# Optimization experiments

Hardware: AMD Instinct MI355X
Metric: run time of the kernel (lower is better)

## Reference

```python
import jax, jax.numpy as jnp
import numpy as np

NUM_NODES = 100000
NUM_FEATS = 128
NUM_EDGES = 3200000
NUM_HEADS = 4


def setup_inputs() -> dict:
    key = jax.random.key(0)
    k1, k2, k3, k4 = jax.random.split(key, 4)
    x = jax.random.normal(k1, (NUM_NODES, NUM_FEATS), dtype=jnp.float32)
    # torch Linear: weight [out, in], bias [out]; scale weight down so q.k scores stay sane
    W = jax.random.normal(k2, (2 * NUM_HEADS * NUM_FEATS, NUM_FEATS), dtype=jnp.float32) * 0.05
    b = jax.random.normal(k3, (2 * NUM_HEADS * NUM_FEATS,), dtype=jnp.float32) * 0.05
    edge_index = jax.random.randint(k4, (2, NUM_EDGES), 0, NUM_NODES, dtype=jnp.int64)
    return {"x": x, "W": W, "b": b, "edge_index": edge_index}


def reference(x, W, b, edge_index):
    N = x.shape[0]
    H, F = NUM_HEADS, NUM_FEATS
    # qk_lin: [N, 2*H*F]
    qk = x @ W.T + b
    # 'L (h hdim) -> L h hdim' with hdim=2F, then split along hdim into q, k
    qk = qk.reshape(N, H, 2 * F)
    q = qk[..., :F]   # [N, H, F]
    k = qk[..., F:]   # [N, H, F]
    row, col = edge_index[0], edge_index[1]
    # per-edge dot-product score per head (NOTE: original never applies self.scale)
    scores = jnp.einsum('ehf,ehf->eh', q[row], k[col])  # [E, H]
    # sparse softmax over columns within each (head, row) segment
    seg_max = jax.ops.segment_max(scores, row, num_segments=N)  # [N, H]
    ex = jnp.exp(scores - seg_max[row])
    seg_sum = jax.ops.segment_sum(ex, row, num_segments=N)      # [N, H]
    attn = ex / seg_sum[row]                                    # [E, H]
    # average over heads (torch.sparse.sum over head dim / num_heads)
    return attn.mean(axis=1)                                    # [E] per-edge values
```

## Files before the change

### kernel.cpp

```cpp
#include <hip/hip_runtime.h>
#include <hip/hip_fp16.h>

#define N_NODES 100000
#define N_FEATS 128
#define N_EDGES 3200000
#define N_HEADS 4
#define QK_HALFS ((size_t)N_NODES * 512)
#define CAP 64
#define GROUPS 8
#define ROWS_PER_G (N_NODES / GROUPS)
#define STRIPS (N_NODES / 16)
#define NBLK ((N_NODES + 255) / 256)
#define XCONV_BLKS 6250
#define WCONV_BLKS 64
#define GEMM3_BLKS 6250

typedef _Float16 half2t __attribute__((ext_vector_type(2)));
typedef _Float16 fp16x8 __attribute__((ext_vector_type(8)));
typedef float f32x4 __attribute__((ext_vector_type(4)));
struct alignas(16) H8 { half2t h[4]; };
union F4H8 { f32x4 f; H8 h; };

__device__ inline float fdot2(half2t a, half2t b, float c) {
#if __has_builtin(__builtin_amdgcn_fdot2)
  return __builtin_amdgcn_fdot2(a, b, c, false);
#else
  return c + (float)a.x * (float)b.x + (float)a.y * (float)b.y;
#endif
}

__device__ inline float dotH8(const H8& a, const H8& b, float c) {
  c = fdot2(a.h[0], b.h[0], c);
  c = fdot2(a.h[1], b.h[1], c);
  c = fdot2(a.h[2], b.h[2], c);
  c = fdot2(a.h[3], b.h[3], c);
  return c;
}

__device__ inline H8 cvt8nt(const float* p) {
  f32x4 f0 = __builtin_nontemporal_load((const f32x4*)p);
  f32x4 f1 = __builtin_nontemporal_load((const f32x4*)(p + 4));
  H8 h;
  h.h[0] = (half2t){(_Float16)f0[0], (_Float16)f0[1]};
  h.h[1] = (half2t){(_Float16)f0[2], (_Float16)f0[3]};
  h.h[2] = (half2t){(_Float16)f1[0], (_Float16)f1[1]};
  h.h[3] = (half2t){(_Float16)f1[2], (_Float16)f1[3]};
  return h;
}

__global__ __launch_bounds__(256) void prep(const float* __restrict__ x,
                                            const float* __restrict__ W,
                                            _Float16* __restrict__ xh,
                                            _Float16* __restrict__ wh,
                                            int* __restrict__ cnt) {
  int bid = blockIdx.x;
  if (bid < XCONV_BLKS) {
    size_t base = (size_t)bid * 2048 + threadIdx.x * 8;
    H8 h = cvt8nt(x + base);
    *(H8*)(xh + base) = h;
  } else if (bid < XCONV_BLKS + WCONV_BLKS) {
    size_t base = (size_t)(bid - XCONV_BLKS) * 2048 + threadIdx.x * 8;
    H8 h = cvt8nt(W + base);
    *(H8*)(wh + base) = h;
  } else {
    int i = (bid - XCONV_BLKS - WCONV_BLKS) * 256 + threadIdx.x;
    if (i < N_NODES) cnt[i] = 0;
  }
}

__global__ __launch_bounds__(256) void gemm_qk3(const _Float16* __restrict__ xh,
                                                const _Float16* __restrict__ wh,
                                                const float* __restrict__ bias,
                                                __half* __restrict__ qh,
                                                __half* __restrict__ kh) {
  const int wave = threadIdx.x >> 6;
  const int wid = blockIdx.x * 4 + wave;
  const int ctp = wid / STRIPS;
  const int strip = wid % STRIPS;
  const int m0 = strip * 16;
  const int lane = threadIdx.x & 63;
  const int ml = lane & 15, quad = lane >> 4;
  const _Float16* xr = xh + (size_t)(m0 + ml) * 128 + quad * 8;
  const _Float16* wr0 = wh + (size_t)(ctp * 256 + ml) * 128 + quad * 8;
  const _Float16* wr1 = wr0 + (size_t)128 * 128;
  f32x4 acc0[8] = {}, acc1[8] = {};
#pragma unroll
  for (int kk = 0; kk < 4; kk++) {
    fp16x8 a = *(const fp16x8*)(xr + kk * 32);
#pragma unroll
    for (int t = 0; t < 8; t++) {
      fp16x8 b0 = *(const fp16x8*)(wr0 + (size_t)t * 2048 + kk * 32);
      acc0[t] = __builtin_amdgcn_mfma_f32_16x16x32_f16(a, b0, acc0[t], 0, 0, 0);
    }
#pragma unroll
    for (int t = 0; t < 8; t++) {
      fp16x8 b1 = *(const fp16x8*)(wr1 + (size_t)t * 2048 + kk * 32);
      acc1[t] = __builtin_amdgcn_mfma_f32_16x16x32_f16(a, b1, acc1[t], 0, 0, 0);
    }
  }
  float bv0[8], bv1[8];
#pragma unroll
  for (int t = 0; t < 8; t++) {
    bv0[t] = bias[ctp * 256 + t * 16 + ml];
    bv1[t] = bias[ctp * 256 + 128 + t * 16 + ml];
  }
#pragma unroll
  for (int r = 0; r < 4; r++) {
    F4H8 pq, pk;
#pragma unroll
    for (int t = 0; t < 4; t++) {
      pq.h.h[t] = (half2t){(_Float16)(acc0[2 * t][r] + bv0[2 * t]),
                           (_Float16)(acc0[2 * t + 1][r] + bv0[2 * t + 1])};
      pk.h.h[t] = (half2t){(_Float16)(acc1[2 * t][r] + bv1[2 * t]),
                           (_Float16)(acc1[2 * t + 1][r] + bv1[2 * t + 1])};
    }
    size_t gbase = (size_t)(m0 + quad * 4 + r) * 512 + ctp * 128 + ml * 8;
    __builtin_nontemporal_store(pq.f, (f32x4*)((__half*)qh + gbase));
    __builtin_nontemporal_store(pk.f, (f32x4*)((__half*)kh + gbase));
  }
}

__global__ __launch_bounds__(256) void scatter_slot(const int* __restrict__ edges,
                                                    int* __restrict__ cnt,
                                                    int2* __restrict__ ceS) {
  const int g = blockIdx.x & 7;
  const int sub = blockIdx.x >> 3;
  const int nsub = gridDim.x >> 3;
  const int rlo = g * ROWS_PER_G, rhi = rlo + ROWS_PER_G;
  for (int base = sub * 256; base < N_EDGES; base += nsub * 256) {
    int e = base + threadIdx.x;
    int r = __builtin_nontemporal_load(&edges[e]);
    if (r >= rlo && r < rhi) {
      int p = atomicAdd(&cnt[r], 1);
      int c = __builtin_nontemporal_load(&edges[N_EDGES + e]);
      if (p < CAP) ceS[r * CAP + p] = make_int2(c, e);
    }
  }
}

__global__ __launch_bounds__(256) void attn_slot(const __half* __restrict__ qp,
                                                 const __half* __restrict__ kp,
                                                 const int* __restrict__ cnt,
                                                 const int2* __restrict__ ceS,
                                                 float* __restrict__ out) {
  __shared__ float4 sc[4][CAP];
  const int wave = threadIdx.x >> 6;
  const int lane = threadIdx.x & 63;
  const int g = lane >> 4, l = lane & 15;
  const int n = blockIdx.x * 4 + wave;
  if (n >= N_NODES) return;
  const int deg = cnt[n];
  if (deg <= 0) return;
  const int dmin = deg < CAP ? deg : CAP;
  const int sbase = n * CAP;

  int ca = 0, eb = 0;
  if (lane < dmin) {
    int2 ce = ceS[sbase + lane];
    ca = ce.x;
    eb = ce.y;
  }

  H8 qv[4];
  {
    const f32x4* qr = (const f32x4*)(qp + (size_t)n * 512);
#pragma unroll
    for (int j = 0; j < 4; j++) {
      F4H8 u;
      u.f = __builtin_nontemporal_load(qr + j * 16 + l);
      qv[j] = u.h;
    }
  }

  for (int i0 = 0; i0 < dmin; i0 += 16) {
    int col[4]; bool act[4]; int ii[4];
#pragma unroll
    for (int u = 0; u < 4; u++) {
      ii[u] = i0 + u * 4 + g;
      act[u] = ii[u] < dmin;
      col[u] = __shfl(ca, ii[u] & 63);
    }
    H8 kv[4][4];
#pragma unroll
    for (int u = 0; u < 4; u++) {
      const H8* kr = (const H8*)(kp + (size_t)col[u] * 512);
#pragma unroll
      for (int j = 0; j < 4; j++) kv[u][j] = kr[j * 16 + l];
    }
    float a[4][4];
#pragma unroll
    for (int u = 0; u < 4; u++)
#pragma unroll
      for (int j = 0; j < 4; j++) a[u][j] = dotH8(kv[u][j], qv[j], 0.f);
#pragma unroll
    for (int u = 0; u < 4; u++)
#pragma unroll
      for (int o = 1; o < 16; o <<= 1) {
        a[u][0] += __shfl_xor(a[u][0], o);
        a[u][1] += __shfl_xor(a[u][1], o);
        a[u][2] += __shfl_xor(a[u][2], o);
        a[u][3] += __shfl_xor(a[u][3], o);
      }
#pragma unroll
    for (int u = 0; u < 4; u++)
      if (l == 0 && act[u])
        sc[wave][ii[u]] = make_float4(a[u][0], a[u][1], a[u][2], a[u][3]);
  }
  __threadfence_block();

  float mx0 = -1e30f, mx1 = -1e30f, mx2 = -1e30f, mx3 = -1e30f;
  for (int i = lane; i < dmin; i += 64) {
    float4 v = sc[wave][i];
    mx0 = fmaxf(mx0, v.x); mx1 = fmaxf(mx1, v.y);
    mx2 = fmaxf(mx2, v.z); mx3 = fmaxf(mx3, v.w);
  }
#pragma unroll
  for (int o = 32; o > 0; o >>= 1) {
    mx0 = fmaxf(mx0, __shfl_xor(mx0, o));
    mx1 = fmaxf(mx1, __shfl_xor(mx1, o));
    mx2 = fmaxf(mx2, __shfl_xor(mx2, o));
    mx3 = fmaxf(mx3, __shfl_xor(mx3, o));
  }
  float sm0 = 0.f, sm1 = 0.f, sm2 = 0.f, sm3 = 0.f;
  for (int i = lane; i < dmin; i += 64) {
    float4 v = sc[wave][i];
    float4 e;
    e.x = __expf(v.x - mx0); e.y = __expf(v.y - mx1);
    e.z = __expf(v.z - mx2); e.w = __expf(v.w - mx3);
    sc[wave][i] = e;
    sm0 += e.x; sm1 += e.y; sm2 += e.z; sm3 += e.w;
  }
#pragma unroll
  for (int o = 32; o > 0; o >>= 1) {
    sm0 += __shfl_xor(sm0, o);
    sm1 += __shfl_xor(sm1, o);
    sm2 += __shfl_xor(sm2, o);
    sm3 += __shfl_xor(sm3, o);
  }
  float rs0 = 1.f / sm0, rs1 = 1.f / sm1, rs2 = 1.f / sm2, rs3 = 1.f / sm3;
  if (lane < dmin) {
    float4 e = sc[wave][lane];
    float w = 0.25f * (e.x * rs0 + e.y * rs1) + 0.25f * (e.z * rs2 + e.w * rs3);
    out[eb] = w;
  }
}

extern "C" void kernel_launch(void* const* d_in, const int* in_sizes, int n_in,
                              void* d_out, int out_size, void* d_ws, size_t ws_size,
                              hipStream_t stream) {
  const float* x = (const float*)d_in[0];
  const float* W = (const float*)d_in[1];
  const float* b = (const float*)d_in[2];
  const int* edges = (const int*)d_in[3];
  float* out = (float*)d_out;

  char* ws = (char*)d_ws;
  size_t o = 0;
  __half* qh = (__half*)(ws + o); o += QK_HALFS * 2;
  __half* kh = (__half*)(ws + o); o += QK_HALFS * 2;
  int* cnt    = (int*)(ws + o); o += (size_t)N_NODES * 4;
  _Float16* wh = (_Float16*)(ws + o); o += (size_t)2 * N_HEADS * 128 * 128 * 2;
  int2* ceS   = (int2*)(ws + o); o += (size_t)N_NODES * CAP * 8;
  _Float16* xh = (_Float16*)ceS;
  (void)ws_size; (void)in_sizes; (void)n_in; (void)out_size;

  prep<<<dim3(XCONV_BLKS + WCONV_BLKS + NBLK), dim3(256), 0, stream>>>(
      x, W, xh, wh, cnt);
  gemm_qk3<<<dim3(GEMM3_BLKS), dim3(256), 0, stream>>>(xh, wh, b, qh, kh);
  scatter_slot<<<dim3(4096), dim3(256), 0, stream>>>(edges, cnt, ceS);
  attn_slot<<<dim3((N_NODES + 3) / 4), dim3(256), 0, stream>>>(
      qh, kh, cnt, ceS, out);
}
```

Before: 919.1 us.

## Fuse x fp16 conversion into GEMM and merge W conversion with edge scatter

Removes the separate x-to-fp16 prep pass: the GEMM now loads fp32 x directly and converts to fp16 in registers before the MFMA. The W conversion blocks are appended to the scatter kernel, and the counter zeroing becomes a hipMemsetAsync. This drops a full write and read of the fp16 copy of x (about 25 MB each way) and one launch. In exchange, each GEMM wave reads fp32 x, which is twice the bytes of the old fp16 copy and is re-read once per column tile.

```diff
diff --git a/kernel.cpp b/kernel.cpp
--- a/kernel.cpp
+++ b/kernel.cpp
@@ -10,8 +10,8 @@
 #define GROUPS 8
 #define ROWS_PER_G (N_NODES / GROUPS)
 #define STRIPS (N_NODES / 16)
-#define NBLK ((N_NODES + 255) / 256)
-#define XCONV_BLKS 6250
+#define SCAT_BLKS 4096
+#define SCAT_NSUB 512
 #define WCONV_BLKS 64
 #define GEMM3_BLKS 6250
 
@@ -48,27 +48,44 @@
   return h;
 }
 
-__global__ __launch_bounds__(256) void prep(const float* __restrict__ x,
-                                            const float* __restrict__ W,
-                                            _Float16* __restrict__ xh,
-                                            _Float16* __restrict__ wh,
-                                            int* __restrict__ cnt) {
-  int bid = blockIdx.x;
-  if (bid < XCONV_BLKS) {
-    size_t base = (size_t)bid * 2048 + threadIdx.x * 8;
-    H8 h = cvt8nt(x + base);
-    *(H8*)(xh + base) = h;
-  } else if (bid < XCONV_BLKS + WCONV_BLKS) {
-    size_t base = (size_t)(bid - XCONV_BLKS) * 2048 + threadIdx.x * 8;
+__device__ inline fp16x8 cvt8f(const float* p) {
+  f32x4 f0 = *(const f32x4*)p;
+  f32x4 f1 = *(const f32x4*)(p + 4);
+  fp16x8 a;
+  a[0] = (_Float16)f0[0]; a[1] = (_Float16)f0[1];
+  a[2] = (_Float16)f0[2]; a[3] = (_Float16)f0[3];
+  a[4] = (_Float16)f1[0]; a[5] = (_Float16)f1[1];
+  a[6] = (_Float16)f1[2]; a[7] = (_Float16)f1[3];
+  return a;
+}
+
+__global__ __launch_bounds__(256) void scatter_wcvt(const int* __restrict__ edges,
+                                                    int* __restrict__ cnt,
+                                                    int2* __restrict__ ceS,
+                                                    const float* __restrict__ W,
+                                                    _Float16* __restrict__ wh) {
+  const int bid = blockIdx.x;
+  if (bid >= SCAT_BLKS) {
+    size_t base = (size_t)(bid - SCAT_BLKS) * 2048 + threadIdx.x * 8;
     H8 h = cvt8nt(W + base);
     *(H8*)(wh + base) = h;
-  } else {
-    int i = (bid - XCONV_BLKS - WCONV_BLKS) * 256 + threadIdx.x;
-    if (i < N_NODES) cnt[i] = 0;
-  }
-}
-
-__global__ __launch_bounds__(256) void gemm_qk3(const _Float16* __restrict__ xh,
+    return;
+  }
+  const int g = bid & 7;
+  const int sub = bid >> 3;
+  const int rlo = g * ROWS_PER_G, rhi = rlo + ROWS_PER_G;
+  for (int base = sub * 256; base < N_EDGES; base += SCAT_NSUB * 256) {
+    int e = base + threadIdx.x;
+    int r = __builtin_nontemporal_load(&edges[e]);
+    if (r >= rlo && r < rhi) {
+      int p = atomicAdd(&cnt[r], 1);
+      int c = __builtin_nontemporal_load(&edges[N_EDGES + e]);
+      if (p < CAP) ceS[r * CAP + p] = make_int2(c, e);
+    }
+  }
+}
+
+__global__ __launch_bounds__(256) void gemm_qk5(const float* __restrict__ x,
                                                 const _Float16* __restrict__ wh,
                                                 const float* __restrict__ bias,
                                                 __half* __restrict__ qh,
@@ -80,13 +97,13 @@
   const int m0 = strip * 16;
   const int lane = threadIdx.x & 63;
   const int ml = lane & 15, quad = lane >> 4;
-  const _Float16* xr = xh + (size_t)(m0 + ml) * 128 + quad * 8;
+  const float* xr = x + (size_t)(m0 + ml) * 128 + quad * 8;
   const _Float16* wr0 = wh + (size_t)(ctp * 256 + ml) * 128 + quad * 8;
   const _Float16* wr1 = wr0 + (size_t)128 * 128;
   f32x4 acc0[8] = {}, acc1[8] = {};
 #pragma unroll
   for (int kk = 0; kk < 4; kk++) {
-    fp16x8 a = *(const fp16x8*)(xr + kk * 32);
+    fp16x8 a = cvt8f(xr + kk * 32);
 #pragma unroll
     for (int t = 0; t < 8; t++) {
       fp16x8 b0 = *(const fp16x8*)(wr0 + (size_t)t * 2048 + kk * 32);
@@ -117,24 +134,6 @@
     size_t gbase = (size_t)(m0 + quad * 4 + r) * 512 + ctp * 128 + ml * 8;
     __builtin_nontemporal_store(pq.f, (f32x4*)((__half*)qh + gbase));
     __builtin_nontemporal_store(pk.f, (f32x4*)((__half*)kh + gbase));
-  }
-}
-
-__global__ __launch_bounds__(256) void scatter_slot(const int* __restrict__ edges,
-                                                    int* __restrict__ cnt,
-                                                    int2* __restrict__ ceS) {
-  const int g = blockIdx.x & 7;
-  const int sub = blockIdx.x >> 3;
-  const int nsub = gridDim.x >> 3;
-  const int rlo = g * ROWS_PER_G, rhi = rlo + ROWS_PER_G;
-  for (int base = sub * 256; base < N_EDGES; base += nsub * 256) {
-    int e = base + threadIdx.x;
-    int r = __builtin_nontemporal_load(&edges[e]);
-    if (r >= rlo && r < rhi) {
-      int p = atomicAdd(&cnt[r], 1);
-      int c = __builtin_nontemporal_load(&edges[N_EDGES + e]);
-      if (p < CAP) ceS[r * CAP + p] = make_int2(c, e);
-    }
   }
 }
 
@@ -261,13 +260,12 @@
   int* cnt    = (int*)(ws + o); o += (size_t)N_NODES * 4;
   _Float16* wh = (_Float16*)(ws + o); o += (size_t)2 * N_HEADS * 128 * 128 * 2;
   int2* ceS   = (int2*)(ws + o); o += (size_t)N_NODES * CAP * 8;
-  _Float16* xh = (_Float16*)ceS;
   (void)ws_size; (void)in_sizes; (void)n_in; (void)out_size;
 
-  prep<<<dim3(XCONV_BLKS + WCONV_BLKS + NBLK), dim3(256), 0, stream>>>(
-      x, W, xh, wh, cnt);
-  gemm_qk3<<<dim3(GEMM3_BLKS), dim3(256), 0, stream>>>(xh, wh, b, qh, kh);
-  scatter_slot<<<dim3(4096), dim3(256), 0, stream>>>(edges, cnt, ceS);
+  hipMemsetAsync(cnt, 0, (size_t)N_NODES * 4, stream);
+  scatter_wcvt<<<dim3(SCAT_BLKS + WCONV_BLKS), dim3(256), 0, stream>>>(
+      edges, cnt, ceS, W, wh);
+  gemm_qk5<<<dim3(GEMM3_BLKS), dim3(256), 0, stream>>>(x, wh, b, qh, kh);
   attn_slot<<<dim3((N_NODES + 3) / 4), dim3(256), 0, stream>>>(
       qh, kh, cnt, ceS, out);
 }
```

New measurement: 926.8 us. About the same (+0.8%).
